# Kernel optimization log

Hardware: AMD Instinct MI355X
Metric: run time of the kernel (lower is better)

Reference implementation:

```python
import jax, jax.numpy as jnp
import numpy as np

N = 50000      # nodes
E = 600000     # edges (avg degree 12)
D_IN = 32      # Processor hard-codes first GBlock in_channels=32
D_H = 128      # args.d_hidden
N_MID = 3      # n_mp - 1 = layers after the first (2 skip + 1 no-skip)


def setup_inputs() -> dict:
    key = jax.random.key(0)
    ks = jax.random.split(key, 10)
    s_in = 1.0 / np.sqrt(D_IN)
    s_h = 1.0 / np.sqrt(D_H)
    return {
        "z": jax.random.normal(ks[0], (N, D_IN), jnp.float32),
        "edge_index": jax.random.randint(ks[1], (2, E), 0, N, dtype=jnp.int32),
        "edge_weight": jax.random.uniform(ks[2], (E,), jnp.float32),
        "batch": jnp.zeros((N,), jnp.int32),
        # first GBlock (32 -> 128)
        "W_rel0": jax.random.normal(ks[3], (D_H, D_IN), jnp.float32) * s_in,
        "b_rel0": jax.random.normal(ks[4], (D_H,), jnp.float32) * 0.01,
        "W_root0": jax.random.normal(ks[5], (D_H, D_IN), jnp.float32) * s_in,
        # remaining 3 GBlocks (128 -> 128), stacked
        "W_rel": jax.random.normal(ks[6], (N_MID, D_H, D_H), jnp.float32) * s_h,
        "b_rel": jax.random.normal(ks[7], (N_MID, D_H), jnp.float32) * 0.01,
        "W_root": jax.random.normal(ks[8], (N_MID, D_H, D_H), jnp.float32) * s_h,
    }


def graph_conv(x, src, dst, w, W_rel, b_rel, W_root):
    # PyG GraphConv: lin_rel(sum_{j->i} w_e * x_j) + lin_root(x)
    msg = x[src] * w[:, None]                                   # [E, d] gather
    agg = jax.ops.segment_sum(msg, dst, num_segments=x.shape[0])  # [N, d] scatter-add
    return agg @ W_rel.T + b_rel + x @ W_root.T


def reference(z, edge_index, edge_weight, batch, W_rel0, b_rel0, W_root0, W_rel, b_rel, W_root):
    src, dst = edge_index[0], edge_index[1]
    # GBlock 0: 32 -> 128, norm=Identity, no skip
    out = jax.nn.relu(graph_conv(z, src, dst, edge_weight, W_rel0, b_rel0, W_root0))
    # GBlocks 1..2 with residual+relu, GBlock 3 without
    skips = (True, True, False)
    for i, skip in enumerate(skips):
        h = jax.nn.relu(graph_conv(out, src, dst, edge_weight, W_rel[i], b_rel[i], W_root[i]))
        out = jax.nn.relu(h + out) if skip else h
    # dropout with p=0.0 (eval) is identity
    return out
```

## Files before the change

kernel.cpp:

```cpp
#include <hip/hip_runtime.h>

#define N_NODES 50000
#define N_EDGES 600000
#define D_IN 32
#define D_H 128
#define CAP 64
#define GPC 391

typedef __attribute__((ext_vector_type(8))) short short8;
typedef __attribute__((ext_vector_type(4))) float f32x4;
typedef __attribute__((ext_vector_type(4))) unsigned int u32x4;

static inline int cdiv(int a, int b) { return (a + b - 1) / b; }

__device__ inline unsigned short f2bf(float f) {
    unsigned int b = __float_as_uint(f);
    return (unsigned short)((b + 0x7FFFu + ((b >> 16) & 1u)) >> 16);
}
__device__ inline unsigned int pack_bf16(float a, float b) {
    return (unsigned int)f2bf(a) | ((unsigned int)f2bf(b) << 16);
}
__device__ inline float bf_lo(unsigned int u) { return __uint_as_float(u << 16); }
__device__ inline float bf_hi(unsigned int u) { return __uint_as_float(u & 0xFFFF0000u); }


__global__ __launch_bounds__(256) void prep_kernel(
    const float* __restrict__ z, unsigned int* __restrict__ zbf,
    const float* __restrict__ Wrel0, const float* __restrict__ Wroot0,
    const float* __restrict__ Wrel, const float* __restrict__ Wroot,
    unsigned short* __restrict__ W0, unsigned short* __restrict__ W1,
    int* __restrict__ cnt) {
    int i = blockIdx.x * 256 + threadIdx.x;
    if (i < N_NODES) cnt[i] = 0;
    if (i < N_NODES * D_IN / 4) {
        float4 v = ((const float4*)z)[i];
        ((uint2*)zbf)[i] = make_uint2(pack_bf16(v.x, v.y), pack_bf16(v.z, v.w));
    }
    if (i < 128 * 64) {
        int o = i >> 6, k = i & 63;
        float v = (k < 32) ? Wrel0[o * 32 + k] : Wroot0[o * 32 + (k - 32)];
        W0[i] = f2bf(v);
    }
    if (i < 3 * 128 * 256) {
        int L = i >> 15;
        int r = i & 32767;
        int o = r >> 8, k = r & 255;
        float v = (k < 128) ? Wrel[L * 16384 + o * 128 + k]
                            : Wroot[L * 16384 + o * 128 + (k - 128)];
        W1[i] = f2bf(v);
    }
}


__global__ void fillpad_kernel(const int* __restrict__ src, const int* __restrict__ dst,
                               const float* __restrict__ w, int* __restrict__ cnt,
                               unsigned int* __restrict__ ep, int e) {
    int i = blockIdx.x * blockDim.x + threadIdx.x;
    if (i < e) {
        int d = dst[i];
        int slot = atomicAdd(&cnt[d], 1);
        if (slot < CAP) {
            unsigned int v = (unsigned int)src[i] | ((unsigned int)f2bf(w[i]) << 16);
            __builtin_nontemporal_store(v, ep + (size_t)d * CAP + slot);
        }
    }
}


__global__ __launch_bounds__(256) void agg128_kernel(
    const unsigned int* __restrict__ xc, const int* __restrict__ cnt,
    const unsigned int* __restrict__ ep, unsigned int* __restrict__ aggc, int n) {
    int b = blockIdx.x;
    int xcd = b & 7, g = b >> 3;
    int c = xcd >> 1, half = xcd & 1;
    int ng = half * GPC + g;
    int tid = threadIdx.x;
    int node = ng * 64 + (tid >> 2);
    int s = tid & 3;
    if (node >= n) return;
    int deg = cnt[node]; if (deg > CAP) deg = CAP;
    const u32x4* X4 = (const u32x4*)xc;
    const size_t cbase = (size_t)c * N_NODES;
    const unsigned int* row = ep + (size_t)node * CAP;
    float a0 = 0.f, a1 = 0.f, a2 = 0.f, a3 = 0.f,
          a4 = 0.f, a5 = 0.f, a6 = 0.f, a7 = 0.f;
    int j = 0;
    for (; j + 4 <= deg; j += 4) {
        unsigned int e0 = __builtin_nontemporal_load(row + j);
        unsigned int e1 = __builtin_nontemporal_load(row + j + 1);
        unsigned int e2 = __builtin_nontemporal_load(row + j + 2);
        unsigned int e3 = __builtin_nontemporal_load(row + j + 3);
        u32x4 v0 = X4[(cbase + (e0 & 0xFFFFu)) * 4 + s];
        u32x4 v1 = X4[(cbase + (e1 & 0xFFFFu)) * 4 + s];
        u32x4 v2 = X4[(cbase + (e2 & 0xFFFFu)) * 4 + s];
        u32x4 v3 = X4[(cbase + (e3 & 0xFFFFu)) * 4 + s];
        float w0 = bf_hi(e0), w1 = bf_hi(e1), w2 = bf_hi(e2), w3 = bf_hi(e3);
        a0 += bf_lo(v0.x) * w0; a1 += bf_hi(v0.x) * w0; a2 += bf_lo(v0.y) * w0; a3 += bf_hi(v0.y) * w0;
        a4 += bf_lo(v0.z) * w0; a5 += bf_hi(v0.z) * w0; a6 += bf_lo(v0.w) * w0; a7 += bf_hi(v0.w) * w0;
        a0 += bf_lo(v1.x) * w1; a1 += bf_hi(v1.x) * w1; a2 += bf_lo(v1.y) * w1; a3 += bf_hi(v1.y) * w1;
        a4 += bf_lo(v1.z) * w1; a5 += bf_hi(v1.z) * w1; a6 += bf_lo(v1.w) * w1; a7 += bf_hi(v1.w) * w1;
        a0 += bf_lo(v2.x) * w2; a1 += bf_hi(v2.x) * w2; a2 += bf_lo(v2.y) * w2; a3 += bf_hi(v2.y) * w2;
        a4 += bf_lo(v2.z) * w2; a5 += bf_hi(v2.z) * w2; a6 += bf_lo(v2.w) * w2; a7 += bf_hi(v2.w) * w2;
        a0 += bf_lo(v3.x) * w3; a1 += bf_hi(v3.x) * w3; a2 += bf_lo(v3.y) * w3; a3 += bf_hi(v3.y) * w3;
        a4 += bf_lo(v3.z) * w3; a5 += bf_hi(v3.z) * w3; a6 += bf_lo(v3.w) * w3; a7 += bf_hi(v3.w) * w3;
    }
    for (; j < deg; j++) {
        unsigned int e0 = __builtin_nontemporal_load(row + j);
        u32x4 v0 = X4[(cbase + (e0 & 0xFFFFu)) * 4 + s];
        float w0 = bf_hi(e0);
        a0 += bf_lo(v0.x) * w0; a1 += bf_hi(v0.x) * w0; a2 += bf_lo(v0.y) * w0; a3 += bf_hi(v0.y) * w0;
        a4 += bf_lo(v0.z) * w0; a5 += bf_hi(v0.z) * w0; a6 += bf_lo(v0.w) * w0; a7 += bf_hi(v0.w) * w0;
    }
    u32x4 r = (u32x4){pack_bf16(a0, a1), pack_bf16(a2, a3),
                      pack_bf16(a4, a5), pack_bf16(a6, a7)};
    __builtin_nontemporal_store(r, (u32x4*)aggc + (cbase + node) * 4 + s);
}


__global__ __launch_bounds__(256) void agg32_kernel(
    const unsigned int* __restrict__ zbf, const int* __restrict__ cnt,
    const unsigned int* __restrict__ ep, unsigned int* __restrict__ aggbf, int n) {
    int tid = threadIdx.x;
    int wid = tid >> 6, l = tid & 63;
    int sub = l >> 4, q = l & 15;
    int node = blockIdx.x * 16 + wid * 4 + sub;
    if (node >= n) return;
    int deg = cnt[node]; if (deg > CAP) deg = CAP;
    const unsigned int* row = ep + (size_t)node * CAP;
    float a0 = 0.f, a1 = 0.f;
    int j = 0;
    for (; j + 4 <= deg; j += 4) {
        unsigned int e0 = __builtin_nontemporal_load(row + j);
        unsigned int e1 = __builtin_nontemporal_load(row + j + 1);
        unsigned int e2 = __builtin_nontemporal_load(row + j + 2);
        unsigned int e3 = __builtin_nontemporal_load(row + j + 3);
        unsigned int v0 = zbf[(size_t)(e0 & 0xFFFFu) * 16 + q];
        unsigned int v1 = zbf[(size_t)(e1 & 0xFFFFu) * 16 + q];
        unsigned int v2 = zbf[(size_t)(e2 & 0xFFFFu) * 16 + q];
        unsigned int v3 = zbf[(size_t)(e3 & 0xFFFFu) * 16 + q];
        float w0 = bf_hi(e0), w1 = bf_hi(e1), w2 = bf_hi(e2), w3 = bf_hi(e3);
        a0 += bf_lo(v0) * w0; a1 += bf_hi(v0) * w0;
        a0 += bf_lo(v1) * w1; a1 += bf_hi(v1) * w1;
        a0 += bf_lo(v2) * w2; a1 += bf_hi(v2) * w2;
        a0 += bf_lo(v3) * w3; a1 += bf_hi(v3) * w3;
    }
    for (; j < deg; j++) {
        unsigned int e0 = __builtin_nontemporal_load(row + j);
        unsigned int v0 = zbf[(size_t)(e0 & 0xFFFFu) * 16 + q];
        float w0 = bf_hi(e0);
        a0 += bf_lo(v0) * w0; a1 += bf_hi(v0) * w0;
    }
    aggbf[(size_t)node * 16 + q] = pack_bf16(a0, a1);
}


template <int KH, bool SKIP, bool FINAL>
__global__ __launch_bounds__(256) void lin_kernel(
    const unsigned short* __restrict__ agg, const unsigned short* __restrict__ x,
    const unsigned short* __restrict__ W2, const float* __restrict__ bias,
    void* __restrict__ outv, int n) {
    constexpr int K2 = 2 * KH;
    constexpr int NKS = K2 / 32;
    constexpr int LOGNKS = (NKS == 2) ? 1 : 3;
    constexpr int SLOTS = 16 * K2;
    __shared__ uint2 Abuf[SLOTS];
    const int tid = threadIdx.x;
    const int n0 = blockIdx.x * 64;

#pragma unroll
    for (int it = 0; it < SLOTS / 256; it++) {
        int d = tid + it * 256;
        int jh = d & 1;
        int l = (d >> 1) & 63;
        int ks = (d >> 7) & (NKS - 1);
        int mt = d >> (7 + LOGNKS);
        int r = mt * 16 + (l & 15);
        int k = ks * 32 + ((l >> 4) << 3) + jh * 4;
        int node = n0 + r;
        uint2 v = make_uint2(0u, 0u);
        if (node < n) {
            int kk = (k < KH) ? k : (k - KH);
            const unsigned short* base = (k < KH) ? agg : x;
            size_t addr;
            if (KH == 128)
                addr = ((size_t)(kk >> 5) * N_NODES + node) * 32 + (kk & 31);
            else
                addr = (size_t)node * KH + kk;
            v = *(const uint2*)(base + addr);
        }
        Abuf[d] = v;
    }
    __syncthreads();

    const int w = tid >> 6, l = tid & 63;
    const int lo16 = l & 15, hi = l >> 4;

    f32x4 acc[4][2];
#pragma unroll
    for (int nt = 0; nt < 2; nt++) {
        float bv = bias[w * 32 + nt * 16 + lo16];
#pragma unroll
        for (int mt = 0; mt < 4; mt++) acc[mt][nt] = (f32x4){bv, bv, bv, bv};
    }

    const short8* Afr = (const short8*)Abuf;
#pragma unroll
    for (int ks = 0; ks < NKS; ks++) {
        short8 bfr[2];
#pragma unroll
        for (int nt = 0; nt < 2; nt++) {
            int o = w * 32 + nt * 16 + lo16;
            bfr[nt] = *(const short8*)(W2 + (size_t)o * K2 + ks * 32 + hi * 8);
        }
#pragma unroll
        for (int mt = 0; mt < 4; mt++) {
            short8 afr = Afr[(mt * NKS + ks) * 64 + l];
            acc[mt][0] = __builtin_amdgcn_mfma_f32_16x16x32_bf16(afr, bfr[0], acc[mt][0], 0, 0, 0);
            acc[mt][1] = __builtin_amdgcn_mfma_f32_16x16x32_bf16(afr, bfr[1], acc[mt][1], 0, 0, 0);
        }
    }

    const unsigned short* Au16 = (const unsigned short*)Abuf;
#pragma unroll
    for (int mt = 0; mt < 4; mt++) {
#pragma unroll
        for (int j = 0; j < 4; j++) {
            int node = n0 + mt * 16 + hi * 4 + j;
            if (node < n) {
#pragma unroll
                for (int nt = 0; nt < 2; nt++) {
                    int o = w * 32 + nt * 16 + lo16;
                    float v = acc[mt][nt][j];
                    v = fmaxf(v, 0.f);
                    if (SKIP) {
                        int us = (((mt * NKS + 4 + w) * 64 + (nt * 2 + (lo16 >> 3)) * 16 + hi * 4 + j) * 2
                                  + ((lo16 >> 2) & 1)) * 4 + (lo16 & 3);
                        float xr = __uint_as_float((unsigned int)Au16[us] << 16);
                        v = fmaxf(v + xr, 0.f);
                    }
                    if (FINAL) {
                        ((float*)outv)[(size_t)node * D_H + o] = v;
                    } else {
                        ((unsigned short*)outv)[((size_t)w * N_NODES + node) * 32 + nt * 16 + lo16] = f2bf(v);
                    }
                }
            }
        }
    }
}


extern "C" void kernel_launch(void* const* d_in, const int* in_sizes, int n_in,
                              void* d_out, int out_size, void* d_ws, size_t ws_size,
                              hipStream_t stream) {
    const float* z      = (const float*)d_in[0];
    const int*   eidx   = (const int*)d_in[1];
    const float* ew     = (const float*)d_in[2];
    const float* Wrel0  = (const float*)d_in[4];
    const float* brel0  = (const float*)d_in[5];
    const float* Wroot0 = (const float*)d_in[6];
    const float* Wrel   = (const float*)d_in[7];
    const float* brel   = (const float*)d_in[8];
    const float* Wroot  = (const float*)d_in[9];

    const int* src = eidx;
    const int* dst = eidx + N_EDGES;

    char* p = (char*)d_ws;
    auto alloc = [&](size_t bytes) {
        void* r = (void*)p;
        p += (bytes + 255) & ~(size_t)255;
        return r;
    };
    int*   cnt    = (int*)alloc((size_t)N_NODES * 4);
    unsigned int* epack = (unsigned int*)alloc((size_t)N_NODES * CAP * 4);
    unsigned int* zbf = (unsigned int*)alloc((size_t)N_NODES * D_IN * 2);
    unsigned int* agg = (unsigned int*)alloc((size_t)N_NODES * D_H * 2);
    unsigned int* h0  = (unsigned int*)alloc((size_t)N_NODES * D_H * 2);
    unsigned int* h1  = (unsigned int*)alloc((size_t)N_NODES * D_H * 2);
    unsigned short* W0bf = (unsigned short*)alloc((size_t)128 * 64 * 2);
    unsigned short* W1bf = (unsigned short*)alloc((size_t)3 * 128 * 256 * 2);
    float* outp = (float*)d_out;

    prep_kernel<<<cdiv(N_NODES * D_IN / 4, 256), 256, 0, stream>>>(
        z, zbf, Wrel0, Wroot0, Wrel, Wroot, W0bf, W1bf, cnt);

    fillpad_kernel<<<cdiv(N_EDGES, 256), 256, 0, stream>>>(src, dst, ew, cnt, epack, N_EDGES);

    const int agg128Grid = 8 * GPC;
    const int agg32Grid  = cdiv(N_NODES, 16);
    const int linGrid    = cdiv(N_NODES, 64);

    agg32_kernel<<<agg32Grid, 256, 0, stream>>>(zbf, cnt, epack, agg, N_NODES);
    lin_kernel<32, false, false><<<linGrid, 256, 0, stream>>>(
        (const unsigned short*)agg, (const unsigned short*)zbf, W0bf, brel0, h0, N_NODES);
    agg128_kernel<<<agg128Grid, 256, 0, stream>>>(h0, cnt, epack, agg, N_NODES);
    lin_kernel<128, true, false><<<linGrid, 256, 0, stream>>>(
        (const unsigned short*)agg, (const unsigned short*)h0, W1bf, brel, h1, N_NODES);
    agg128_kernel<<<agg128Grid, 256, 0, stream>>>(h1, cnt, epack, agg, N_NODES);
    lin_kernel<128, true, false><<<linGrid, 256, 0, stream>>>(
        (const unsigned short*)agg, (const unsigned short*)h1, W1bf + 32768, brel + 128, h0, N_NODES);
    agg128_kernel<<<agg128Grid, 256, 0, stream>>>(h0, cnt, epack, agg, N_NODES);
    lin_kernel<128, false, true><<<linGrid, 256, 0, stream>>>(
        (const unsigned short*)agg, (const unsigned short*)h0, W1bf + 65536, brel + 256, outp, N_NODES);
}
```

Baseline: 239.4 us.

## Switch hidden features from XCD-chunked layout to plain row-major bf16

Replaces the 4-chunk feature layout, whose chunks were each paired with XCDs for L2 locality, with a contiguous [N,128] bf16 layout. Aggregation now maps 16 lanes per node over a full 256-byte row, and the linear kernel reads and writes row-major. The intent is simpler, fully coalesced row gathers and stores. In exchange it loses the per-XCD L2 working-set reduction, so random gathers span the whole feature matrix from every XCD. Also makes the agg32 output store nontemporal.

```diff
diff --git a/kernel.cpp b/kernel.cpp
--- a/kernel.cpp
+++ b/kernel.cpp
@@ -5,7 +5,6 @@
 #define D_IN 32
 #define D_H 128
 #define CAP 64
-#define GPC 391
 
 typedef __attribute__((ext_vector_type(8))) short short8;
 typedef __attribute__((ext_vector_type(4))) float f32x4;
@@ -68,19 +67,15 @@
 
 
 __global__ __launch_bounds__(256) void agg128_kernel(
-    const unsigned int* __restrict__ xc, const int* __restrict__ cnt,
-    const unsigned int* __restrict__ ep, unsigned int* __restrict__ aggc, int n) {
-    int b = blockIdx.x;
-    int xcd = b & 7, g = b >> 3;
-    int c = xcd >> 1, half = xcd & 1;
-    int ng = half * GPC + g;
+    const unsigned int* __restrict__ xbf, const int* __restrict__ cnt,
+    const unsigned int* __restrict__ ep, unsigned int* __restrict__ aggbf, int n) {
     int tid = threadIdx.x;
-    int node = ng * 64 + (tid >> 2);
-    int s = tid & 3;
+    int wid = tid >> 6, l = tid & 63;
+    int sub = l >> 4, q = l & 15;
+    int node = blockIdx.x * 16 + wid * 4 + sub;
     if (node >= n) return;
     int deg = cnt[node]; if (deg > CAP) deg = CAP;
-    const u32x4* X4 = (const u32x4*)xc;
-    const size_t cbase = (size_t)c * N_NODES;
+    const u32x4* X4 = (const u32x4*)xbf;
     const unsigned int* row = ep + (size_t)node * CAP;
     float a0 = 0.f, a1 = 0.f, a2 = 0.f, a3 = 0.f,
           a4 = 0.f, a5 = 0.f, a6 = 0.f, a7 = 0.f;
@@ -90,10 +85,10 @@
         unsigned int e1 = __builtin_nontemporal_load(row + j + 1);
         unsigned int e2 = __builtin_nontemporal_load(row + j + 2);
         unsigned int e3 = __builtin_nontemporal_load(row + j + 3);
-        u32x4 v0 = X4[(cbase + (e0 & 0xFFFFu)) * 4 + s];
-        u32x4 v1 = X4[(cbase + (e1 & 0xFFFFu)) * 4 + s];
-        u32x4 v2 = X4[(cbase + (e2 & 0xFFFFu)) * 4 + s];
-        u32x4 v3 = X4[(cbase + (e3 & 0xFFFFu)) * 4 + s];
+        u32x4 v0 = X4[(size_t)(e0 & 0xFFFFu) * 16 + q];
+        u32x4 v1 = X4[(size_t)(e1 & 0xFFFFu) * 16 + q];
+        u32x4 v2 = X4[(size_t)(e2 & 0xFFFFu) * 16 + q];
+        u32x4 v3 = X4[(size_t)(e3 & 0xFFFFu) * 16 + q];
         float w0 = bf_hi(e0), w1 = bf_hi(e1), w2 = bf_hi(e2), w3 = bf_hi(e3);
         a0 += bf_lo(v0.x) * w0; a1 += bf_hi(v0.x) * w0; a2 += bf_lo(v0.y) * w0; a3 += bf_hi(v0.y) * w0;
         a4 += bf_lo(v0.z) * w0; a5 += bf_hi(v0.z) * w0; a6 += bf_lo(v0.w) * w0; a7 += bf_hi(v0.w) * w0;
@@ -106,16 +101,15 @@
     }
     for (; j < deg; j++) {
         unsigned int e0 = __builtin_nontemporal_load(row + j);
-        u32x4 v0 = X4[(cbase + (e0 & 0xFFFFu)) * 4 + s];
+        u32x4 v0 = X4[(size_t)(e0 & 0xFFFFu) * 16 + q];
         float w0 = bf_hi(e0);
         a0 += bf_lo(v0.x) * w0; a1 += bf_hi(v0.x) * w0; a2 += bf_lo(v0.y) * w0; a3 += bf_hi(v0.y) * w0;
         a4 += bf_lo(v0.z) * w0; a5 += bf_hi(v0.z) * w0; a6 += bf_lo(v0.w) * w0; a7 += bf_hi(v0.w) * w0;
     }
     u32x4 r = (u32x4){pack_bf16(a0, a1), pack_bf16(a2, a3),
                       pack_bf16(a4, a5), pack_bf16(a6, a7)};
-    __builtin_nontemporal_store(r, (u32x4*)aggc + (cbase + node) * 4 + s);
-}
-
+    __builtin_nontemporal_store(r, (u32x4*)aggbf + (size_t)node * 16 + q);
+}
 
 __global__ __launch_bounds__(256) void agg32_kernel(
     const unsigned int* __restrict__ zbf, const int* __restrict__ cnt,
@@ -150,7 +144,7 @@
         float w0 = bf_hi(e0);
         a0 += bf_lo(v0) * w0; a1 += bf_hi(v0) * w0;
     }
-    aggbf[(size_t)node * 16 + q] = pack_bf16(a0, a1);
+    __builtin_nontemporal_store(pack_bf16(a0, a1), aggbf + (size_t)node * 16 + q);
 }
 
 
@@ -179,14 +173,8 @@
         int node = n0 + r;
         uint2 v = make_uint2(0u, 0u);
         if (node < n) {
-            int kk = (k < KH) ? k : (k - KH);
-            const unsigned short* base = (k < KH) ? agg : x;
-            size_t addr;
-            if (KH == 128)
-                addr = ((size_t)(kk >> 5) * N_NODES + node) * 32 + (kk & 31);
-            else
-                addr = (size_t)node * KH + kk;
-            v = *(const uint2*)(base + addr);
+            v = (k < KH) ? *(const uint2*)(agg + (size_t)node * KH + k)
+                         : *(const uint2*)(x + (size_t)node * KH + (k - KH));
         }
         Abuf[d] = v;
     }
@@ -238,11 +226,10 @@
                         float xr = __uint_as_float((unsigned int)Au16[us] << 16);
                         v = fmaxf(v + xr, 0.f);
                     }
-                    if (FINAL) {
+                    if (FINAL)
                         ((float*)outv)[(size_t)node * D_H + o] = v;
-                    } else {
-                        ((unsigned short*)outv)[((size_t)w * N_NODES + node) * 32 + nt * 16 + lo16] = f2bf(v);
-                    }
+                    else
+                        ((unsigned short*)outv)[(size_t)node * D_H + o] = f2bf(v);
                 }
             }
         }
@@ -287,20 +274,19 @@
 
     fillpad_kernel<<<cdiv(N_EDGES, 256), 256, 0, stream>>>(src, dst, ew, cnt, epack, N_EDGES);
 
-    const int agg128Grid = 8 * GPC;
-    const int agg32Grid  = cdiv(N_NODES, 16);
-    const int linGrid    = cdiv(N_NODES, 64);
-
-    agg32_kernel<<<agg32Grid, 256, 0, stream>>>(zbf, cnt, epack, agg, N_NODES);
+    const int aggGrid = cdiv(N_NODES, 16);
+    const int linGrid = cdiv(N_NODES, 64);
+
+    agg32_kernel<<<aggGrid, 256, 0, stream>>>(zbf, cnt, epack, agg, N_NODES);
     lin_kernel<32, false, false><<<linGrid, 256, 0, stream>>>(
         (const unsigned short*)agg, (const unsigned short*)zbf, W0bf, brel0, h0, N_NODES);
-    agg128_kernel<<<agg128Grid, 256, 0, stream>>>(h0, cnt, epack, agg, N_NODES);
+    agg128_kernel<<<aggGrid, 256, 0, stream>>>(h0, cnt, epack, agg, N_NODES);
     lin_kernel<128, true, false><<<linGrid, 256, 0, stream>>>(
         (const unsigned short*)agg, (const unsigned short*)h0, W1bf, brel, h1, N_NODES);
-    agg128_kernel<<<agg128Grid, 256, 0, stream>>>(h1, cnt, epack, agg, N_NODES);
+    agg128_kernel<<<aggGrid, 256, 0, stream>>>(h1, cnt, epack, agg, N_NODES);
     lin_kernel<128, true, false><<<linGrid, 256, 0, stream>>>(
         (const unsigned short*)agg, (const unsigned short*)h1, W1bf + 32768, brel + 128, h0, N_NODES);
-    agg128_kernel<<<agg128Grid, 256, 0, stream>>>(h0, cnt, epack, agg, N_NODES);
+    agg128_kernel<<<aggGrid, 256, 0, stream>>>(h0, cnt, epack, agg, N_NODES);
     lin_kernel<128, false, true><<<linGrid, 256, 0, stream>>>(
         (const unsigned short*)agg, (const unsigned short*)h0, W1bf + 65536, brel + 256, outp, N_NODES);
 }
```

New measurement: 209.9 us. 12.3% less time.
